# Kernel tuning notes

Measured on AMD Instinct MI355X. Metric: run time of the kernel, lower is better.

## Reference

```python
import jax, jax.numpy as jnp
import numpy as np

_CONST = 10000.0
D = 128
L = 8192
N = 32


def setup_inputs() -> dict:
    key = jax.random.key(0)
    X = jax.random.normal(key, (N, D, L), dtype=jnp.float32)
    return {"X": X}


def reference(X: jnp.ndarray) -> jnp.ndarray:
    # X: [N, D, L]; pairs (i, i + D//2) rotated by angle k * theta_i at position k.
    d = X.shape[1]
    half = d // 2
    i = jnp.arange(half, dtype=jnp.float32)              # [D/2]
    theta = _CONST ** (2.0 * i / d)                      # [D/2]  (faithful: positive exponent)
    k = jnp.arange(X.shape[2], dtype=jnp.float32)        # [L]
    angles = theta[:, None] * k[None, :]                 # [D/2, L]
    c = jnp.cos(angles)[None, :, :]                      # [1, D/2, L]
    s = jnp.sin(angles)[None, :, :]
    x1 = X[:, :half, :]                                  # [N, D/2, L]
    x2 = X[:, half:, :]
    out1 = c * x1 - s * x2
    out2 = s * x1 + c * x2
    return jnp.concatenate([out1, out2], axis=1)         # [N, D, L]
```

## Files before the change

kernel.cpp:

```cpp
#include <hip/hip_runtime.h>
#include <math.h>

#define N_BATCH 32
#define D_DIM   128
#define HALF    64
#define SEQ_L   8192
#define L_VEC4  (SEQ_L / 4)
#define TAB_ELEMS (HALF * SEQ_L)
#define TAB_BYTES (TAB_ELEMS * 2 * sizeof(float))

__global__ void rope_tables(float* __restrict__ ctab, float* __restrict__ stab) {
    int idx = blockIdx.x * blockDim.x + threadIdx.x;
    if (idx >= TAB_ELEMS) return;
    int i = idx >> 13;
    int k = idx & (SEQ_L - 1);
    float theta = (float)pow(10000.0, (double)i * (1.0 / 64.0));
    float angle = theta * (float)k;
    float s, c;
    sincosf(angle, &s, &c);
    ctab[idx] = c;
    stab[idx] = s;
}

__global__ void rope_apply(const float4* __restrict__ X,
                           float4* __restrict__ out,
                           const float4* __restrict__ ctab,
                           const float4* __restrict__ stab) {
    int tid = blockIdx.x * blockDim.x + threadIdx.x;
    if (tid >= N_BATCH * HALF * L_VEC4) return;
    int k4 = tid & (L_VEC4 - 1);
    int i  = (tid >> 11) & (HALF - 1);
    int n  = tid >> 17;

    int tidx = (i << 11) + k4;
    float4 c = ctab[tidx];
    float4 s = stab[tidx];
    int base1 = ((n * D_DIM + i) << 11) + k4;
    int base2 = ((n * D_DIM + i + HALF) << 11) + k4;
    float4 x1 = X[base1];
    float4 x2 = X[base2];

    float4 o1, o2;
    o1.x = c.x * x1.x - s.x * x2.x;  o2.x = s.x * x1.x + c.x * x2.x;
    o1.y = c.y * x1.y - s.y * x2.y;  o2.y = s.y * x1.y + c.y * x2.y;
    o1.z = c.z * x1.z - s.z * x2.z;  o2.z = s.z * x1.z + c.z * x2.z;
    o1.w = c.w * x1.w - s.w * x2.w;  o2.w = s.w * x1.w + c.w * x2.w;

    out[base1] = o1;
    out[base2] = o2;
}

__global__ void rope_apply_inline(const float4* __restrict__ X,
                                  float4* __restrict__ out) {
    int tid = blockIdx.x * blockDim.x + threadIdx.x;
    if (tid >= N_BATCH * HALF * L_VEC4) return;
    int k4 = tid & (L_VEC4 - 1);
    int i  = (tid >> 11) & (HALF - 1);
    int n  = tid >> 17;

    float theta = (float)pow(10000.0, (double)i * (1.0 / 64.0));
    float4 c, s;
    {
        float k0 = (float)(k4 * 4);
        sincosf(theta * k0,          &s.x, &c.x);
        sincosf(theta * (k0 + 1.0f), &s.y, &c.y);
        sincosf(theta * (k0 + 2.0f), &s.z, &c.z);
        sincosf(theta * (k0 + 3.0f), &s.w, &c.w);
    }
    int base1 = ((n * D_DIM + i) << 11) + k4;
    int base2 = ((n * D_DIM + i + HALF) << 11) + k4;
    float4 x1 = X[base1];
    float4 x2 = X[base2];
    float4 o1, o2;
    o1.x = c.x * x1.x - s.x * x2.x;  o2.x = s.x * x1.x + c.x * x2.x;
    o1.y = c.y * x1.y - s.y * x2.y;  o2.y = s.y * x1.y + c.y * x2.y;
    o1.z = c.z * x1.z - s.z * x2.z;  o2.z = s.z * x1.z + c.z * x2.z;
    o1.w = c.w * x1.w - s.w * x2.w;  o2.w = s.w * x1.w + c.w * x2.w;
    out[base1] = o1;
    out[base2] = o2;
}

extern "C" void kernel_launch(void* const* d_in, const int* in_sizes, int n_in,
                              void* d_out, int out_size, void* d_ws, size_t ws_size,
                              hipStream_t stream) {
    const float4* X  = (const float4*)d_in[0];
    float4* out      = (float4*)d_out;

    const int apply_threads = N_BATCH * HALF * L_VEC4;
    const int block = 256;

    if (ws_size >= TAB_BYTES) {
        float* ctab = (float*)d_ws;
        float* stab = ctab + TAB_ELEMS;
        rope_tables<<<(TAB_ELEMS + block - 1) / block, block, 0, stream>>>(ctab, stab);
        rope_apply<<<(apply_threads + block - 1) / block, block, 0, stream>>>(
            X, out, (const float4*)ctab, (const float4*)stab);
    } else {
        rope_apply_inline<<<(apply_threads + block - 1) / block, block, 0, stream>>>(X, out);
    }
}
```

Baseline: 51.11 us.

## Fuse table generation into apply and reuse sincos across batch groups

Drops the precomputed cos/sin table kernel and the table reads. Each thread now computes its four sincos values once and applies them to 8 batch elements in an unrolled loop. This removes a kernel launch and the table memory traffic, and spreads the trig cost over 8 batches. In exchange the grid has 8x fewer threads, each doing more serial memory work, which could reduce memory-level parallelism.

Result: faster. 44.39 us (-13.1%).

```diff
diff --git a/kernel.cpp b/kernel.cpp
--- a/kernel.cpp
+++ b/kernel.cpp
@@ -1,101 +1,56 @@
 #include <hip/hip_runtime.h>
 #include <math.h>
+
 
 #define N_BATCH 32
 #define D_DIM   128
 #define HALF    64
 #define SEQ_L   8192
 #define L_VEC4  (SEQ_L / 4)
-#define TAB_ELEMS (HALF * SEQ_L)
-#define TAB_BYTES (TAB_ELEMS * 2 * sizeof(float))
+#define NN      8
+#define NGRP    (N_BATCH / NN)
+#define TOTAL_THREADS (NGRP * HALF * L_VEC4)
 
-__global__ void rope_tables(float* __restrict__ ctab, float* __restrict__ stab) {
-    int idx = blockIdx.x * blockDim.x + threadIdx.x;
-    if (idx >= TAB_ELEMS) return;
-    int i = idx >> 13;
-    int k = idx & (SEQ_L - 1);
-    float theta = (float)pow(10000.0, (double)i * (1.0 / 64.0));
-    float angle = theta * (float)k;
-    float s, c;
-    sincosf(angle, &s, &c);
-    ctab[idx] = c;
-    stab[idx] = s;
-}
-
-__global__ void rope_apply(const float4* __restrict__ X,
-                           float4* __restrict__ out,
-                           const float4* __restrict__ ctab,
-                           const float4* __restrict__ stab) {
+__global__ __launch_bounds__(256) void rope_fused(const float4* __restrict__ X,
+                                                  float4* __restrict__ out) {
     int tid = blockIdx.x * blockDim.x + threadIdx.x;
-    if (tid >= N_BATCH * HALF * L_VEC4) return;
+    if (tid >= TOTAL_THREADS) return;
     int k4 = tid & (L_VEC4 - 1);
     int i  = (tid >> 11) & (HALF - 1);
-    int n  = tid >> 17;
-
-    int tidx = (i << 11) + k4;
-    float4 c = ctab[tidx];
-    float4 s = stab[tidx];
-    int base1 = ((n * D_DIM + i) << 11) + k4;
-    int base2 = ((n * D_DIM + i + HALF) << 11) + k4;
-    float4 x1 = X[base1];
-    float4 x2 = X[base2];
-
-    float4 o1, o2;
-    o1.x = c.x * x1.x - s.x * x2.x;  o2.x = s.x * x1.x + c.x * x2.x;
-    o1.y = c.y * x1.y - s.y * x2.y;  o2.y = s.y * x1.y + c.y * x2.y;
-    o1.z = c.z * x1.z - s.z * x2.z;  o2.z = s.z * x1.z + c.z * x2.z;
-    o1.w = c.w * x1.w - s.w * x2.w;  o2.w = s.w * x1.w + c.w * x2.w;
-
-    out[base1] = o1;
-    out[base2] = o2;
-}
-
-__global__ void rope_apply_inline(const float4* __restrict__ X,
-                                  float4* __restrict__ out) {
-    int tid = blockIdx.x * blockDim.x + threadIdx.x;
-    if (tid >= N_BATCH * HALF * L_VEC4) return;
-    int k4 = tid & (L_VEC4 - 1);
-    int i  = (tid >> 11) & (HALF - 1);
-    int n  = tid >> 17;
+    int g  = tid >> 17;
 
     float theta = (float)pow(10000.0, (double)i * (1.0 / 64.0));
+
+    float k0 = (float)(k4 * 4);
     float4 c, s;
-    {
-        float k0 = (float)(k4 * 4);
-        sincosf(theta * k0,          &s.x, &c.x);
-        sincosf(theta * (k0 + 1.0f), &s.y, &c.y);
-        sincosf(theta * (k0 + 2.0f), &s.z, &c.z);
-        sincosf(theta * (k0 + 3.0f), &s.w, &c.w);
+    sincosf(theta * k0,          &s.x, &c.x);
+    sincosf(theta * (k0 + 1.0f), &s.y, &c.y);
+    sincosf(theta * (k0 + 2.0f), &s.z, &c.z);
+    sincosf(theta * (k0 + 3.0f), &s.w, &c.w);
+
+    int n0 = g * NN;
+    #pragma unroll
+    for (int t = 0; t < NN; ++t) {
+        int n = n0 + t;
+        int b1 = ((n * D_DIM + i) << 11) + k4;
+        int b2 = b1 + (HALF << 11);
+        float4 x1 = X[b1];
+        float4 x2 = X[b2];
+        float4 o1, o2;
+        o1.x = c.x * x1.x - s.x * x2.x;  o2.x = s.x * x1.x + c.x * x2.x;
+        o1.y = c.y * x1.y - s.y * x2.y;  o2.y = s.y * x1.y + c.y * x2.y;
+        o1.z = c.z * x1.z - s.z * x2.z;  o2.z = s.z * x1.z + c.z * x2.z;
+        o1.w = c.w * x1.w - s.w * x2.w;  o2.w = s.w * x1.w + c.w * x2.w;
+        out[b1] = o1;
+        out[b2] = o2;
     }
-    int base1 = ((n * D_DIM + i) << 11) + k4;
-    int base2 = ((n * D_DIM + i + HALF) << 11) + k4;
-    float4 x1 = X[base1];
-    float4 x2 = X[base2];
-    float4 o1, o2;
-    o1.x = c.x * x1.x - s.x * x2.x;  o2.x = s.x * x1.x + c.x * x2.x;
-    o1.y = c.y * x1.y - s.y * x2.y;  o2.y = s.y * x1.y + c.y * x2.y;
-    o1.z = c.z * x1.z - s.z * x2.z;  o2.z = s.z * x1.z + c.z * x2.z;
-    o1.w = c.w * x1.w - s.w * x2.w;  o2.w = s.w * x1.w + c.w * x2.w;
-    out[base1] = o1;
-    out[base2] = o2;
 }
 
 extern "C" void kernel_launch(void* const* d_in, const int* in_sizes, int n_in,
                               void* d_out, int out_size, void* d_ws, size_t ws_size,
                               hipStream_t stream) {
-    const float4* X  = (const float4*)d_in[0];
-    float4* out      = (float4*)d_out;
-
-    const int apply_threads = N_BATCH * HALF * L_VEC4;
+    const float4* X = (const float4*)d_in[0];
+    float4* out     = (float4*)d_out;
     const int block = 256;
-
-    if (ws_size >= TAB_BYTES) {
-        float* ctab = (float*)d_ws;
-        float* stab = ctab + TAB_ELEMS;
-        rope_tables<<<(TAB_ELEMS + block - 1) / block, block, 0, stream>>>(ctab, stab);
-        rope_apply<<<(apply_threads + block - 1) / block, block, 0, stream>>>(
-            X, out, (const float4*)ctab, (const float4*)stab);
-    } else {
-        rope_apply_inline<<<(apply_threads + block - 1) / block, block, 0, stream>>>(X, out);
-    }
+    rope_fused<<<TOTAL_THREADS / block, block, 0, stream>>>(X, out);
 }
```
